# Kernel optimization log

Hardware: AMD Instinct MI355X
Metric: run time of the kernel (lower is better)

The kernel has to match this reference:

```python
import jax, jax.numpy as jnp
import numpy as np

H = 8   # num_heads
D = 64  # out_features per head

def setup_inputs() -> dict:
    key = jax.random.key(0)
    k1, k2, k3, k4 = jax.random.split(key, 4)
    B, N, F_IN, E = 2, 8192, 512, 65536
    x = jax.random.normal(k1, (B, N, F_IN), dtype=jnp.float32)
    edge_indices = jax.random.randint(k2, (2, E), 0, N)
    W = jax.random.normal(k3, (H * D, F_IN), dtype=jnp.float32) * (1.0 / np.sqrt(F_IN))
    a = jax.random.normal(k4, (2 * D, 1), dtype=jnp.float32) * 0.1
    return {"x": x, "edge_indices": edge_indices, "W": W, "a": a}

def reference(x, edge_indices, W, a):
    # Faithful translation of GraphAttentionLayer.forward (eval mode: dropout = identity).
    B, N, _ = x.shape
    h = (x @ W.T).reshape(B, N, H, D)              # [B,N,H,D]
    src, dst = edge_indices[0], edge_indices[1]
    E = src.shape[0]
    h_src = h[:, src]                               # [B,E,H,D]
    h_dst = h[:, dst]                               # [B,E,H,D]
    # cat([h_src,h_dst]) @ a  ==  h_src @ a[:D] + h_dst @ a[D:]
    a1, a2 = a[:D, 0], a[D:, 0]
    scores = jnp.einsum('behd,d->beh', h_src, a1) + jnp.einsum('behd,d->beh', h_dst, a2)
    scores = jax.nn.leaky_relu(scores, negative_slope=0.2)      # [B,E,H]
    # NOTE: original code softmaxes over the BATCH dim (dim=0) per edge.
    sm = jax.nn.softmax(scores, axis=0)                          # [B,E,H]
    last_edge = jnp.full((N,), -1, dtype=jnp.int32).at[src].max(
        jnp.arange(E, dtype=jnp.int32))                          # [N]
    has_edge = last_edge >= 0
    w = jnp.where(has_edge[None, :, None],
                  sm[:, jnp.clip(last_edge, 0)], 0.0)            # [B,N,H]
    # aggregated[:, s] += w[:, s, :, None] * h_dst[:, e] for each edge e with src[e]==s
    # (weights fully built before aggregation loop) => w[s] * segment_sum(h_dst over src)
    agg_dst = jnp.zeros((B, N, H, D), dtype=h.dtype).at[:, src].add(h_dst)
    aggregated = w[..., None] * agg_dst                          # [B,N,H,D]
    return aggregated.mean(axis=2)                               # [B,N,D]
```

## Files before the change

kernel.cpp:

```cpp
#include <hip/hip_runtime.h>
#include <stdint.h>

#define H_HEADS 8
#define DDIM 64
#define NNODES 8192
#define BB 2
#define FIN 512
#define FOUT 512
#define EDGES 65536
#define CAP 32

typedef unsigned short u16;
typedef unsigned int u32;
typedef __bf16 bf16x8 __attribute__((ext_vector_type(8)));
typedef float f32x4 __attribute__((ext_vector_type(4)));

__device__ __forceinline__ u16 f2bf(float f) {
    u32 u = __float_as_uint(f);
    return (u16)((u + 0x7FFFu + ((u >> 16) & 1u)) >> 16);
}
__device__ __forceinline__ float bf2f(u32 s) {
    return __uint_as_float(s << 16);
}
__device__ __forceinline__ uint4 pack8(float4 a, float4 b) {
    return make_uint4(f2bf(a.x) | ((u32)f2bf(a.y) << 16),
                      f2bf(a.z) | ((u32)f2bf(a.w) << 16),
                      f2bf(b.x) | ((u32)f2bf(b.y) << 16),
                      f2bf(b.z) | ((u32)f2bf(b.w) << 16));
}

#define NWB (FOUT * FIN / 8 / 256)
#define NEB 64
__global__ __launch_bounds__(256) void prep_kernel(
    const float* __restrict__ W, const int* __restrict__ src,
    const int* __restrict__ dst, u16* __restrict__ Wb,
    int* __restrict__ cursor, int* __restrict__ le_pack,
    int* __restrict__ csr_dst) {
    int blk = blockIdx.x;
    if (blk < NWB) {
        int i = blk * 256 + threadIdx.x;
        const float4* p = (const float4*)W;
        float4 v0 = p[(size_t)i * 2], v1 = p[(size_t)i * 2 + 1];
        ((uint4*)Wb)[i] = pack8(v0, v1);
    } else {
        int t = (blk - NWB) * 256 + threadIdx.x;
#pragma unroll
        for (int k = 0; k < 4; k++) {
            int e = t * 4 + k;
            int s = src[e], d = dst[e];
            int slot = atomicAdd(&cursor[s], 1);
            if (slot < CAP) csr_dst[(size_t)s * CAP + slot] = d;
            atomicMax(&le_pack[s], (e << 13) | d);
        }
    }
}

#define GLDS(g, l)                                                              \
    __builtin_amdgcn_global_load_lds(                                           \
        (const __attribute__((address_space(1))) u32*)(g),                      \
        (__attribute__((address_space(3))) u32*)(l), 16, 0, 0)

__global__ __launch_bounds__(256) void gemm_mfma(const float* __restrict__ X,
                                                 const u16* __restrict__ Bm,
                                                 const float* __restrict__ a,
                                                 u16* __restrict__ C,
                                                 float* __restrict__ s1,
                                                 float* __restrict__ s2) {
    __shared__ u16 As[128 * 32];
    __shared__ u16 Bs[128 * 32];
    int tid = threadIdx.x;
    int gb = blockIdx.x;
    int m_idx = (gb & 7) | ((gb >> 5) << 3);
    int n_idx = (gb >> 3) & 3;
    int m0 = m_idx * 128, n0 = n_idx * 128;
    int lane = tid & 63, wv = tid >> 6;
    int wr = (wv >> 1) * 64, wc = (wv & 1) * 64;
    int l15 = lane & 15, quad = lane >> 4;
    f32x4 acc[4][4] = {};

    float a1v[4], a2v[4];
#pragma unroll
    for (int j = 0; j < 4; j++) {
        a1v[j] = a[j * 16 + l15];
        a2v[j] = a[DDIM + j * 16 + l15];
    }

    int srow = tid >> 2;
    int scol = (tid & 3) * 8;
    const float* Ag = X + (size_t)(m0 + srow) * FIN + scol;
    const u16* Bg = Bm + (size_t)(n0 + srow) * FIN + scol;
    u16* Al = As + tid * 8;
    u16* Bl = Bs + tid * 8;

    for (int k0 = 0; k0 < FIN; k0 += 32) {
        __syncthreads();
        GLDS(Bg + k0, Bl);
        GLDS(Bg + k0 + (size_t)64 * FIN, Bl + 64 * 32);
        float4 fa0 = *(const float4*)(Ag + k0);
        float4 fa1 = *(const float4*)(Ag + k0 + 4);
        float4 fb0 = *(const float4*)(Ag + k0 + (size_t)64 * FIN);
        float4 fb1 = *(const float4*)(Ag + k0 + (size_t)64 * FIN + 4);
        *(uint4*)Al = pack8(fa0, fa1);
        *(uint4*)(Al + 64 * 32) = pack8(fb0, fb1);
        __syncthreads();
        bf16x8 af[4], bfr[4];
#pragma unroll
        for (int i = 0; i < 4; i++)
            af[i] = *(const bf16x8*)(As + (wr + i * 16 + l15) * 32 + quad * 8);
#pragma unroll
        for (int j = 0; j < 4; j++)
            bfr[j] = *(const bf16x8*)(Bs + (wc + j * 16 + l15) * 32 + quad * 8);
#pragma unroll
        for (int i = 0; i < 4; i++)
#pragma unroll
            for (int j = 0; j < 4; j++)
                acc[i][j] = __builtin_amdgcn_mfma_f32_16x16x32_bf16(
                    af[i], bfr[j], acc[i][j], 0, 0, 0);
    }

#pragma unroll
    for (int i = 0; i < 4; i++) {
        int row_base = m0 + wr + i * 16 + quad * 4;
#pragma unroll
        for (int j = 0; j < 4; j++) {
            int col = n0 + wc + j * 16 + l15;
#pragma unroll
            for (int r = 0; r < 4; r++)
                C[(size_t)(row_base + r) * FOUT + col] = f2bf(acc[i][j][r]);
        }
    }

    int head = n_idx * 2 + (wv & 1);
#pragma unroll
    for (int i = 0; i < 4; i++) {
#pragma unroll
        for (int r = 0; r < 4; r++) {
            float p1 = 0.f, p2 = 0.f;
#pragma unroll
            for (int j = 0; j < 4; j++) {
                p1 += a1v[j] * acc[i][j][r];
                p2 += a2v[j] * acc[i][j][r];
            }
#pragma unroll
            for (int m = 1; m <= 8; m <<= 1) {
                p1 += __shfl_xor(p1, m);
                p2 += __shfl_xor(p2, m);
            }
            if (l15 == 0) {
                int row = m0 + wr + i * 16 + quad * 4 + r;
                s1[row * H_HEADS + head] = p1;
                s2[row * H_HEADS + head] = p2;
            }
        }
    }
}

__global__ __launch_bounds__(256) void aggregate(const u16* __restrict__ h,
                                                 const float* __restrict__ s1,
                                                 const float* __restrict__ s2,
                                                 const int* __restrict__ cursor,
                                                 const int* __restrict__ le_pack,
                                                 const int* __restrict__ csr_dst,
                                                 float* __restrict__ out, int N) {
    int n = blockIdx.x * 2 + (threadIdx.x >> 7);
    int b = (threadIdx.x >> 6) & 1;
    int lane = threadIdx.x & 63;
    int head = lane >> 3;

    int deg = cursor[n];
    deg = deg < CAP ? deg : CAP;
    int pk = le_pack[n];

    const int* cp = csr_dst + (size_t)n * CAP;
    int myidx = (lane < CAP) ? cp[lane] : 0;

    float wgt = 0.f;
    if (deg > 0) {
        int dl = pk & 8191;
        float sc0 = s1[(0 * N + n) * H_HEADS + head] +
                    s2[((size_t)0 * N + dl) * H_HEADS + head];
        float sc1 = s1[((size_t)1 * N + n) * H_HEADS + head] +
                    s2[((size_t)1 * N + dl) * H_HEADS + head];
        sc0 = sc0 >= 0.f ? sc0 : 0.2f * sc0;
        sc1 = sc1 >= 0.f ? sc1 : 0.2f * sc1;
        float m = fmaxf(sc0, sc1);
        float e0 = __expf(sc0 - m), e1 = __expf(sc1 - m);
        wgt = (b == 0 ? e0 : e1) / (e0 + e1);
    }

    float acc[8] = {};
    const u16* hb = h + (size_t)b * N * FOUT + lane * 8;
    for (int j0 = 0; j0 < deg; j0 += 4) {
#pragma unroll
        for (int k = 0; k < 4; k++) {
            int j = j0 + k;
            float f = (j < deg) ? 1.0f : 0.0f;
            int dn = (j < deg) ? __shfl(myidx, j) : 0;
            uint4 v = *(const uint4*)(hb + (size_t)dn * FOUT);
            acc[0] = fmaf(f, bf2f(v.x & 0xffffu), acc[0]);
            acc[1] = fmaf(f, bf2f(v.x >> 16), acc[1]);
            acc[2] = fmaf(f, bf2f(v.y & 0xffffu), acc[2]);
            acc[3] = fmaf(f, bf2f(v.y >> 16), acc[3]);
            acc[4] = fmaf(f, bf2f(v.z & 0xffffu), acc[4]);
            acc[5] = fmaf(f, bf2f(v.z >> 16), acc[5]);
            acc[6] = fmaf(f, bf2f(v.w & 0xffffu), acc[6]);
            acc[7] = fmaf(f, bf2f(v.w >> 16), acc[7]);
        }
    }
    float val[8];
#pragma unroll
    for (int k = 0; k < 8; k++) val[k] = acc[k] * wgt;
#pragma unroll
    for (int m = 8; m <= 32; m <<= 1)
#pragma unroll
        for (int k = 0; k < 8; k++) val[k] += __shfl_xor(val[k], m);
    if (lane < 8) {
        float* op = out + ((size_t)b * N + n) * DDIM + lane * 8;
        const float inv = 1.0f / H_HEADS;
        *(float4*)op = make_float4(val[0] * inv, val[1] * inv, val[2] * inv,
                                   val[3] * inv);
        *(float4*)(op + 4) = make_float4(val[4] * inv, val[5] * inv,
                                         val[6] * inv, val[7] * inv);
    }
}

extern "C" void kernel_launch(void* const* d_in, const int* in_sizes, int n_in,
                              void* d_out, int out_size, void* d_ws,
                              size_t ws_size, hipStream_t stream) {
    const float* x = (const float*)d_in[0];
    const int* edges = (const int*)d_in[1];
    const float* W = (const float*)d_in[2];
    const float* a = (const float*)d_in[3];
    float* out = (float*)d_out;

    const int* src = edges;
    const int* dst = edges + EDGES;

    char* p = (char*)d_ws;
    auto carve = [&](size_t bytes) {
        char* r = p;
        p += (bytes + 255) & ~(size_t)255;
        return r;
    };
    u16* Wb = (u16*)carve((size_t)FOUT * FIN * 2);
    u16* h = (u16*)carve((size_t)BB * NNODES * FOUT * 2);
    float* s1 = (float*)carve((size_t)BB * NNODES * H_HEADS * 4);
    float* s2 = (float*)carve((size_t)BB * NNODES * H_HEADS * 4);
    int* cursor = (int*)carve(NNODES * 4);
    int* le_pack = (int*)carve(NNODES * 4);
    int* csr_dst = (int*)carve((size_t)NNODES * CAP * 4);

    const int M = BB * NNODES;

    hipMemsetAsync(cursor, 0, 2 * NNODES * 4, stream);
    prep_kernel<<<NWB + NEB, 256, 0, stream>>>(W, src, dst, Wb, cursor,
                                               le_pack, csr_dst);
    gemm_mfma<<<(M / 128) * (FOUT / 128), 256, 0, stream>>>(x, Wb, a, h, s1,
                                                            s2);
    aggregate<<<NNODES / 2, 256, 0, stream>>>(h, s1, s2, cursor, le_pack,
                                              csr_dst, out, NNODES);
}
```

Baseline: 125.0 us.

## Move edge CSR build into GEMM launch and zero counters in prep kernel

Replaces the hipMemsetAsync with zeroing of cursor/le_pack done by extra blocks in the weight-conversion prep kernel. The edge-bucketing atomics move out of the prep kernel into 64 extra leading blocks of the GEMM launch, so they run concurrently with GEMM tiles. This removes one memset launch and shortens the prep kernel, at the cost of a larger GEMM grid with heterogeneous blocks.

```diff
diff --git a/kernel.cpp b/kernel.cpp
--- a/kernel.cpp
+++ b/kernel.cpp
@@ -9,6 +9,7 @@
 #define FOUT 512
 #define EDGES 65536
 #define CAP 32
+#define NEBLK 64
 
 typedef unsigned short u16;
 typedef unsigned int u32;
@@ -30,12 +31,10 @@
 }
 
 #define NWB (FOUT * FIN / 8 / 256)
-#define NEB 64
-__global__ __launch_bounds__(256) void prep_kernel(
-    const float* __restrict__ W, const int* __restrict__ src,
-    const int* __restrict__ dst, u16* __restrict__ Wb,
-    int* __restrict__ cursor, int* __restrict__ le_pack,
-    int* __restrict__ csr_dst) {
+#define NZB 8
+__global__ __launch_bounds__(256) void prep_kernel(const float* __restrict__ W,
+                                                   u16* __restrict__ Wb,
+                                                   int* __restrict__ zbase) {
     int blk = blockIdx.x;
     if (blk < NWB) {
         int i = blk * 256 + threadIdx.x;
@@ -44,6 +43,29 @@
         ((uint4*)Wb)[i] = pack8(v0, v1);
     } else {
         int t = (blk - NWB) * 256 + threadIdx.x;
+        ((int4*)zbase)[t * 2] = make_int4(0, 0, 0, 0);
+        ((int4*)zbase)[t * 2 + 1] = make_int4(0, 0, 0, 0);
+    }
+}
+
+#define GLDS(g, l)                                                              \
+    __builtin_amdgcn_global_load_lds(                                           \
+        (const __attribute__((address_space(1))) u32*)(g),                      \
+        (__attribute__((address_space(3))) u32*)(l), 16, 0, 0)
+
+__global__ __launch_bounds__(256) void gemm_mfma(
+    const float* __restrict__ X, const u16* __restrict__ Bm,
+    const float* __restrict__ a, const int* __restrict__ src,
+    const int* __restrict__ dst, u16* __restrict__ C, float* __restrict__ s1,
+    float* __restrict__ s2, int* __restrict__ cursor,
+    int* __restrict__ le_pack, int* __restrict__ csr_dst) {
+    __shared__ u16 As[128 * 32];
+    __shared__ u16 Bs[128 * 32];
+    int tid = threadIdx.x;
+    int blk = blockIdx.x;
+
+    if (blk < NEBLK) {
+        int t = blk * 256 + tid;
 #pragma unroll
         for (int k = 0; k < 4; k++) {
             int e = t * 4 + k;
@@ -52,24 +74,10 @@
             if (slot < CAP) csr_dst[(size_t)s * CAP + slot] = d;
             atomicMax(&le_pack[s], (e << 13) | d);
         }
-    }
-}
-
-#define GLDS(g, l)                                                              \
-    __builtin_amdgcn_global_load_lds(                                           \
-        (const __attribute__((address_space(1))) u32*)(g),                      \
-        (__attribute__((address_space(3))) u32*)(l), 16, 0, 0)
-
-__global__ __launch_bounds__(256) void gemm_mfma(const float* __restrict__ X,
-                                                 const u16* __restrict__ Bm,
-                                                 const float* __restrict__ a,
-                                                 u16* __restrict__ C,
-                                                 float* __restrict__ s1,
-                                                 float* __restrict__ s2) {
-    __shared__ u16 As[128 * 32];
-    __shared__ u16 Bs[128 * 32];
-    int tid = threadIdx.x;
-    int gb = blockIdx.x;
+        return;
+    }
+
+    int gb = blk - NEBLK;
     int m_idx = (gb & 7) | ((gb >> 5) << 3);
     int n_idx = (gb >> 3) & 3;
     int m0 = m_idx * 128, n0 = n_idx * 128;
@@ -252,11 +260,9 @@
 
     const int M = BB * NNODES;
 
-    hipMemsetAsync(cursor, 0, 2 * NNODES * 4, stream);
-    prep_kernel<<<NWB + NEB, 256, 0, stream>>>(W, src, dst, Wb, cursor,
-                                               le_pack, csr_dst);
-    gemm_mfma<<<(M / 128) * (FOUT / 128), 256, 0, stream>>>(x, Wb, a, h, s1,
-                                                            s2);
+    prep_kernel<<<NWB + NZB, 256, 0, stream>>>(W, Wb, cursor);
+    gemm_mfma<<<NEBLK + (M / 128) * (FOUT / 128), 256, 0, stream>>>(
+        x, Wb, a, src, dst, h, s1, s2, cursor, le_pack, csr_dst);
     aggregate<<<NNODES / 2, 256, 0, stream>>>(h, s1, s2, cursor, le_pack,
                                               csr_dst, out, NNODES);
 }
```

Measured after the change: 125.1 us. Within noise of the previous version (+0.1%).
